# Kernel tuning notes

Hardware: AMD Instinct MI355X
Metric: run time of the kernel (lower is better)

Reference implementation:

```python
import jax, jax.numpy as jnp
import numpy as np

B, W, H, C = 8, 32, 32, 64   # batch, width, height, hidden_size
NH = 8                        # num_attention_heads
M = 32                        # max_position_embeddings
P = C // 2                    # position_embedding_size (query_positional_score=True)


def setup_inputs() -> dict:
    key = jax.random.key(0)
    ks = jax.random.split(key, 7)
    s = 0.02
    return {
        "hidden_states": jax.random.normal(ks[0], (B, W, H, C), dtype=jnp.float32),
        "row_emb": jax.random.normal(ks[1], (2 * M - 1, P), dtype=jnp.float32) * s,
        "col_emb": jax.random.normal(ks[2], (2 * M - 1, P), dtype=jnp.float32) * s,
        "Wq": jax.random.normal(ks[3], (NH * C, C), dtype=jnp.float32) * s,
        "bq": jnp.zeros((NH * C,), dtype=jnp.float32),
        "Wk": jax.random.normal(ks[4], (NH * C, C), dtype=jnp.float32) * s,
        "bk": jnp.zeros((NH * C,), dtype=jnp.float32),
        "Wv": jax.random.normal(ks[5], (C, NH * C), dtype=jnp.float32) * s,
        "bv": jnp.zeros((C,), dtype=jnp.float32),
    }


def reference(hidden_states, row_emb, col_emb, Wq, bq, Wk, bk, Wv, bv):
    b, w, h, c = hidden_states.shape
    nh = Wq.shape[0] // c
    half = c // 2
    center = row_emb.shape[0] // 2  # = max_position_embeddings - 1

    # projections: all_head_size = nh * c (per source: hidden_size * num_heads)
    q = (hidden_states @ Wq.T + bq).reshape(b, w, h, nh, c)
    k = (hidden_states @ Wk.T + bk).reshape(b, w, h, nh, c)

    # relative index tables: rel[i, j] = (j - i) + (M - 1)
    iw = jnp.arange(w)
    ih = jnp.arange(h)
    rel_w = iw[None, :] - iw[:, None] + center   # (w, w)
    rel_h = ih[None, :] - ih[:, None] + center   # (h, h)
    r_emb = row_emb[rel_w]  # (w, w, P)
    c_emb = col_emb[rel_h]  # (h, h, P)

    # positional scores: q split into row/col halves
    q_row = q[..., :half]
    q_col = q[..., half:]
    row_scores = jnp.einsum('bijhd,ikd->bijhk', q_row, r_emb)  # (b,w,h,nh,w)
    col_scores = jnp.einsum('bijhd,jld->bijhl', q_col, c_emb)  # (b,w,h,nh,h)
    scale = jnp.sqrt(jnp.asarray(c, dtype=hidden_states.dtype))
    scores = (row_scores[..., :, None] + col_scores[..., None, :]) / scale  # (b,w,h,nh,w,h)

    # content scores q^T k
    scores = scores + jnp.einsum('bijhd,bklhd->bijhkl', q, k) / scale

    # softmax over merged spatial key dims (k,l)
    probs = jax.nn.softmax(scores.reshape(b, w, h, nh, w * h), axis=-1).reshape(scores.shape)

    # value mixing directly with hidden_states, then output projection
    mixed = jnp.einsum('bijhkl,bkld->bijhd', probs, hidden_states).reshape(b, w, h, nh * c)
    return mixed @ Wv.T + bv
```

## Files before the change

### kernel.cpp

```cpp
#include <hip/hip_runtime.h>
#include <math.h>

typedef __bf16 bf16;
typedef bf16 bf16x2 __attribute__((ext_vector_type(2)));
typedef bf16 bf16x4 __attribute__((ext_vector_type(4)));
typedef bf16 bf16x8 __attribute__((ext_vector_type(8)));
typedef float f32x4 __attribute__((ext_vector_type(4)));

constexpr int CENTER = 31;

static __device__ __forceinline__ unsigned short f2bf_bits(float f) {
    bf16 b = (bf16)f;
    return __builtin_bit_cast(unsigned short, b);
}

__global__ __launch_bounds__(256)
void prep_kernel(const float* __restrict__ hid,
                 const float* __restrict__ Wq, const float* __restrict__ Wk,
                 const float* __restrict__ Wv,
                 bf16* __restrict__ hb, bf16* __restrict__ htb,
                 bf16* __restrict__ Wqb, bf16* __restrict__ Wkb,
                 bf16* __restrict__ Wvp)
{
    __shared__ __attribute__((aligned(16))) bf16 hs[64][72];

    const int t   = threadIdx.x;
    const int blk = blockIdx.x;
    const int b   = blk >> 4, kc = blk & 15;

    {
        int row = t >> 2, c4 = (t & 3) * 16;
        const float4* src = (const float4*)(hid + ((size_t)b * 1024 + kc * 64 + row) * 64 + c4);
        bf16 tmp[16];
        #pragma unroll
        for (int u = 0; u < 4; ++u) {
            float4 v = src[u];
            tmp[4*u+0] = (bf16)v.x; tmp[4*u+1] = (bf16)v.y;
            tmp[4*u+2] = (bf16)v.z; tmp[4*u+3] = (bf16)v.w;
        }
        *(int4*)&hs[row][c4]     = ((int4*)tmp)[0];
        *(int4*)&hs[row][c4 + 8] = ((int4*)tmp)[1];
        bf16* hdst = hb + ((size_t)b * 1024 + kc * 64 + row) * 64 + c4;
        *(int4*)hdst       = ((int4*)tmp)[0];
        *(int4*)(hdst + 8) = ((int4*)tmp)[1];
    }

    {
        int idx = blk * 256 + t;
        if (idx < 8192) {
            float4 vq = ((const float4*)Wq)[idx];
            float4 vk = ((const float4*)Wk)[idx];
            float4 vv = ((const float4*)Wv)[idx];
            ushort4 pq, pk2, pv;
            pq.x = f2bf_bits(vq.x); pq.y = f2bf_bits(vq.y); pq.z = f2bf_bits(vq.z); pq.w = f2bf_bits(vq.w);
            pk2.x = f2bf_bits(vk.x); pk2.y = f2bf_bits(vk.y); pk2.z = f2bf_bits(vk.z); pk2.w = f2bf_bits(vk.w);
            pv.x = f2bf_bits(vv.x); pv.y = f2bf_bits(vv.y); pv.z = f2bf_bits(vv.z); pv.w = f2bf_bits(vv.w);
            ((ushort4*)Wqb)[idx] = pq;
            ((ushort4*)Wkb)[idx] = pk2;
            int c = idx >> 7, o4 = (idx & 127) * 4;
            size_t dst = (size_t)((c >> 4) * 16 + (o4 >> 5)) * 512 + (c & 15) * 32 + (o4 & 31);
            *(ushort4*)(Wvp + dst) = pv;
        }
    }
    __syncthreads();

    {
        int d = t >> 2, p0 = (t & 3) * 16;
        ushort tmp[16];
        #pragma unroll
        for (int i = 0; i < 16; ++i)
            tmp[i] = __builtin_bit_cast(unsigned short, hs[p0 + i][d]);
        bf16* dst = htb + ((size_t)b * 64 + d) * 1024 + kc * 64 + p0;
        *(int4*)dst       = ((int4*)tmp)[0];
        *(int4*)(dst + 8) = ((int4*)tmp)[1];
    }
}

__global__ __launch_bounds__(256)
void qkproj_kernel(const bf16* __restrict__ hb,
                   const bf16* __restrict__ Wqb, const float* __restrict__ bq,
                   const bf16* __restrict__ Wkb, const float* __restrict__ bk,
                   bf16* __restrict__ qb, bf16* __restrict__ kb)
{
    __shared__ __attribute__((aligned(16))) bf16 As[128][72];
    __shared__ __attribute__((aligned(16))) bf16 Bqs[128][72];
    __shared__ __attribute__((aligned(16))) bf16 Bks[128][72];

    const int t  = threadIdx.x;
    const int pt = blockIdx.x;
    const int ot = blockIdx.y;
    const int p0 = pt * 128;
    const int b  = p0 >> 10;

    {
        int row = t >> 1, ch = (t & 1) * 32;
        const int4* asrc = (const int4*)(hb + (size_t)(p0 + row) * 64 + ch);
        const int4* qsrc = (const int4*)(Wqb + (size_t)(ot * 128 + row) * 64 + ch);
        const int4* ksrc = (const int4*)(Wkb + (size_t)(ot * 128 + row) * 64 + ch);
        #pragma unroll
        for (int u = 0; u < 4; ++u) {
            *(int4*)&As[row][ch + u * 8]  = asrc[u];
            *(int4*)&Bqs[row][ch + u * 8] = qsrc[u];
            *(int4*)&Bks[row][ch + u * 8] = ksrc[u];
        }
    }
    __syncthreads();

    const int w = t >> 6, ln = t & 63, l15 = ln & 15, quad = ln >> 4;

    bf16x8 a[2][2];
    #pragma unroll
    for (int mt = 0; mt < 2; ++mt) {
        a[mt][0] = *(const bf16x8*)&As[w * 32 + mt * 16 + l15][quad * 8];
        a[mt][1] = *(const bf16x8*)&As[w * 32 + mt * 16 + l15][32 + quad * 8];
    }

    const f32x4 z4 = {0.f, 0.f, 0.f, 0.f};

    for (int z = 0; z < 2; ++z) {
        const bf16 (* __restrict__ Bs)[72] = z ? Bks : Bqs;
        const float* bias = z ? bk : bq;
        bf16* outp        = z ? kb : qb;
        const float scale = z ? 1.0f : 0.125f;

        f32x4 acc[2][8];
        #pragma unroll
        for (int mt = 0; mt < 2; ++mt)
            #pragma unroll
            for (int nt = 0; nt < 8; ++nt) acc[mt][nt] = z4;

        #pragma unroll
        for (int nt = 0; nt < 8; ++nt) {
            bf16x8 b0 = *(const bf16x8*)&Bs[nt * 16 + l15][quad * 8];
            bf16x8 b1 = *(const bf16x8*)&Bs[nt * 16 + l15][32 + quad * 8];
            #pragma unroll
            for (int mt = 0; mt < 2; ++mt) {
                acc[mt][nt] = __builtin_amdgcn_mfma_f32_16x16x32_bf16(a[mt][0], b0, acc[mt][nt], 0, 0, 0);
                acc[mt][nt] = __builtin_amdgcn_mfma_f32_16x16x32_bf16(a[mt][1], b1, acc[mt][nt], 0, 0, 0);
            }
        }

        #pragma unroll
        for (int nt = 0; nt < 8; ++nt) {
            int o = ot * 128 + nt * 16 + l15;
            float bv = bias[o];
            int hh = o >> 6, d = o & 63;
            #pragma unroll
            for (int mt = 0; mt < 2; ++mt)
                #pragma unroll
                for (int r = 0; r < 4; ++r) {
                    int pos = (p0 & 1023) + w * 32 + mt * 16 + quad * 4 + r;
                    float val = (acc[mt][nt][r] + bv) * scale;
                    outp[(((size_t)b * 8 + hh) * 1024 + pos) * 64 + d] = (bf16)val;
                }
        }
    }
}

__global__ __launch_bounds__(256)
void bias_kernel(const bf16* __restrict__ qb,
                 const float* __restrict__ row_emb, const float* __restrict__ col_emb,
                 bf16* __restrict__ rowbias, bf16* __restrict__ colbias)
{
    __shared__ __attribute__((aligned(16))) bf16 embRs[63][40];
    __shared__ __attribute__((aligned(16))) bf16 embCs[63][40];

    const int t  = threadIdx.x;
    const int bh = blockIdx.x;
    const int sg = blockIdx.y;

    for (int i = t; i < 2016; i += 256) embRs[i >> 5][i & 31] = (bf16)row_emb[i];
    for (int i = t; i < 2016; i += 256) embCs[i >> 5][i & 31] = (bf16)col_emb[i];
    __syncthreads();

    const int w = t >> 6, ln = t & 63, l15 = ln & 15, quad = ln >> 4;

    #pragma unroll
    for (int u = 0; u < 4; ++u) {
        int s = sg * 16 + u * 4 + w;
        bool cm = s >= 32;
        int ij = cm ? s - 32 : s;

        bf16x8 a[2];
        #pragma unroll
        for (int mt = 0; mt < 2; ++mt) {
            const bf16* ap = cm
                ? qb + ((size_t)bh * 1024 + (mt * 16 + l15) * 32 + ij) * 64 + 32 + quad * 8
                : qb + ((size_t)bh * 1024 + ij * 32 + mt * 16 + l15) * 64 + quad * 8;
            a[mt] = *(const bf16x8*)ap;
        }
        bf16* ob = cm ? colbias : rowbias;

        #pragma unroll
        for (int nt = 0; nt < 2; ++nt) {
            int erow = nt * 16 + l15 + CENTER - ij;
            bf16x8 bfrag = cm ? *(const bf16x8*)&embCs[erow][quad * 8]
                              : *(const bf16x8*)&embRs[erow][quad * 8];
            #pragma unroll
            for (int mt = 0; mt < 2; ++mt) {
                f32x4 c = {0.f, 0.f, 0.f, 0.f};
                c = __builtin_amdgcn_mfma_f32_16x16x32_bf16(a[mt], bfrag, c, 0, 0, 0);
                #pragma unroll
                for (int r = 0; r < 4; ++r) {
                    int ql = mt * 16 + quad * 4 + r;
                    int qrow = cm ? ql * 32 + ij : ij * 32 + ql;
                    ob[((size_t)bh * 1024 + qrow) * 32 + nt * 16 + l15] = (bf16)c[r];
                }
            }
        }
    }
}

__global__ __launch_bounds__(256, 2)
void attn_kernel(const bf16* __restrict__ qb, const bf16* __restrict__ kb,
                 const bf16* __restrict__ htb,
                 const bf16* __restrict__ rowbias, const bf16* __restrict__ colbias,
                 bf16* __restrict__ mixedb)
{
    __shared__ __attribute__((aligned(16))) bf16 Ks[64][72];
    __shared__ __attribute__((aligned(16))) bf16 Hts[64][72];
    __shared__ __attribute__((aligned(16))) bf16 Pp[4][32][72];

    const int t  = threadIdx.x;
    const int qt = blockIdx.x;
    const int bh = blockIdx.y;
    const int b  = bh >> 3, h = bh & 7;
    const int q0 = qt * 128;
    const int w = t >> 6, ln = t & 63, l15 = ln & 15, quad = ln >> 4;

    bf16x8 bq_[2][2];
    float  cbv[2][2][4];
    const bf16* rbp[2];
    #pragma unroll
    for (int mt = 0; mt < 2; ++mt) {
        int qrow = q0 + w * 32 + mt * 16 + l15;
        const bf16* qp = qb + ((size_t)bh * 1024 + qrow) * 64;
        bq_[mt][0] = *(const bf16x8*)(qp + quad * 8);
        bq_[mt][1] = *(const bf16x8*)(qp + 32 + quad * 8);
        #pragma unroll
        for (int par = 0; par < 2; ++par) {
            bf16x4 cv = *(const bf16x4*)(colbias + ((size_t)bh * 1024 + qrow) * 32 + par * 16 + quad * 4);
            #pragma unroll
            for (int r = 0; r < 4; ++r) cbv[mt][par][r] = (float)cv[r];
        }
        rbp[mt] = rowbias + ((size_t)bh * 1024 + qrow) * 32;
    }

    const f32x4 z4 = {0.f, 0.f, 0.f, 0.f};
    f32x4 oacc[2][4];
    float lsum[2] = {0.f, 0.f};
    #pragma unroll
    for (int mt = 0; mt < 2; ++mt)
        #pragma unroll
        for (int dt = 0; dt < 4; ++dt) oacc[mt][dt] = z4;

    bf16* Pw = &Pp[w][0][0];
    const bf16* kcbase = kb + (size_t)bh * 1024 * 64;
    const bf16* hcbase = htb + (size_t)b * 64 * 1024;

    for (int kc = 0; kc < 16; ++kc) {
        __syncthreads();
        {
            int row = t >> 2, c = (t & 3) << 4;
            const bf16* ksrc = kcbase + (size_t)(kc * 64 + row) * 64 + c;
            *(int4*)&Ks[row][c]     = *(const int4*)ksrc;
            *(int4*)&Ks[row][c + 8] = *(const int4*)(ksrc + 8);
            const bf16* hsrc = hcbase + (size_t)row * 1024 + kc * 64 + c;
            *(int4*)&Hts[row][c]     = *(const int4*)hsrc;
            *(int4*)&Hts[row][c + 8] = *(const int4*)(hsrc + 8);
        }
        float rb[2][2];
        #pragma unroll
        for (int mt = 0; mt < 2; ++mt) {
            bf16x2 rv = *(const bf16x2*)(rbp[mt] + kc * 2);
            rb[mt][0] = (float)rv[0]; rb[mt][1] = (float)rv[1];
        }
        __syncthreads();

        f32x4 sf[2][4];
        #pragma unroll
        for (int mt = 0; mt < 2; ++mt)
            #pragma unroll
            for (int kt = 0; kt < 4; ++kt) sf[mt][kt] = z4;
        #pragma unroll
        for (int kt = 0; kt < 4; ++kt) {
            bf16x8 aK0 = *(const bf16x8*)&Ks[kt * 16 + l15][quad * 8];
            bf16x8 aK1 = *(const bf16x8*)&Ks[kt * 16 + l15][32 + quad * 8];
            #pragma unroll
            for (int mt = 0; mt < 2; ++mt) {
                sf[mt][kt] = __builtin_amdgcn_mfma_f32_16x16x32_bf16(aK0, bq_[mt][0], sf[mt][kt], 0, 0, 0);
                sf[mt][kt] = __builtin_amdgcn_mfma_f32_16x16x32_bf16(aK1, bq_[mt][1], sf[mt][kt], 0, 0, 0);
            }
        }

        #pragma unroll
        for (int mt = 0; mt < 2; ++mt)
            #pragma unroll
            for (int kt = 0; kt < 4; ++kt) {
                float rbv = rb[mt][kt >> 1];
                ushort4 pk;
                float p0 = __expf(sf[mt][kt][0] + rbv + cbv[mt][kt & 1][0]);
                float p1 = __expf(sf[mt][kt][1] + rbv + cbv[mt][kt & 1][1]);
                float p2 = __expf(sf[mt][kt][2] + rbv + cbv[mt][kt & 1][2]);
                float p3 = __expf(sf[mt][kt][3] + rbv + cbv[mt][kt & 1][3]);
                lsum[mt] += (p0 + p1) + (p2 + p3);
                pk.x = f2bf_bits(p0); pk.y = f2bf_bits(p1);
                pk.z = f2bf_bits(p2); pk.w = f2bf_bits(p3);
                *(ushort4*)&Pw[(mt * 16 + l15) * 72 + kt * 16 + quad * 4] = pk;
            }

        bf16x8 bp[2][2];
        #pragma unroll
        for (int mt = 0; mt < 2; ++mt) {
            bp[mt][0] = *(const bf16x8*)&Pw[(mt * 16 + l15) * 72 + quad * 8];
            bp[mt][1] = *(const bf16x8*)&Pw[(mt * 16 + l15) * 72 + 32 + quad * 8];
        }
        #pragma unroll
        for (int dt = 0; dt < 4; ++dt) {
            bf16x8 aH0 = *(const bf16x8*)&Hts[dt * 16 + l15][quad * 8];
            bf16x8 aH1 = *(const bf16x8*)&Hts[dt * 16 + l15][32 + quad * 8];
            #pragma unroll
            for (int mt = 0; mt < 2; ++mt) {
                oacc[mt][dt] = __builtin_amdgcn_mfma_f32_16x16x32_bf16(aH0, bp[mt][0], oacc[mt][dt], 0, 0, 0);
                oacc[mt][dt] = __builtin_amdgcn_mfma_f32_16x16x32_bf16(aH1, bp[mt][1], oacc[mt][dt], 0, 0, 0);
            }
        }
    }

    float inv[2];
    #pragma unroll
    for (int mt = 0; mt < 2; ++mt) {
        float v = lsum[mt];
        v += __shfl_xor(v, 16);
        v += __shfl_xor(v, 32);
        inv[mt] = 1.0f / v;
    }
    #pragma unroll
    for (int mt = 0; mt < 2; ++mt) {
        int pos = q0 + w * 32 + mt * 16 + l15;
        bf16* mb = mixedb + ((size_t)b * 1024 + pos) * 512 + h * 64;
        #pragma unroll
        for (int dt = 0; dt < 4; ++dt) {
            ushort4 pk;
            pk.x = f2bf_bits(oacc[mt][dt][0] * inv[mt]);
            pk.y = f2bf_bits(oacc[mt][dt][1] * inv[mt]);
            pk.z = f2bf_bits(oacc[mt][dt][2] * inv[mt]);
            pk.w = f2bf_bits(oacc[mt][dt][3] * inv[mt]);
            *(ushort4*)(mb + dt * 16 + quad * 4) = pk;
        }
    }
}

__global__ __launch_bounds__(256)
void out_proj_kernel(const bf16* __restrict__ mixedb,
                     const bf16* __restrict__ Wvp, const float* __restrict__ bv,
                     float* __restrict__ out)
{
    const int t  = threadIdx.x;
    const int p0 = blockIdx.x * 32;
    const int w = t >> 6, ln = t & 63, l15 = ln & 15, quad = ln >> 4;

    float bvv = bv[w * 16 + l15];
    f32x4 acc[2] = {(f32x4){bvv, bvv, bvv, bvv}, (f32x4){bvv, bvv, bvv, bvv}};

    const bf16* arow0 = mixedb + (size_t)(p0 + l15) * 512 + quad * 8;
    const bf16* arow1 = mixedb + (size_t)(p0 + 16 + l15) * 512 + quad * 8;
    const bf16* bbase = Wvp + (size_t)w * 16 * 512 + l15 * 32 + quad * 8;

    #pragma unroll
    for (int kc = 0; kc < 16; ++kc) {
        bf16x8 a0 = *(const bf16x8*)(arow0 + kc * 32);
        bf16x8 a1 = *(const bf16x8*)(arow1 + kc * 32);
        bf16x8 bfrag = *(const bf16x8*)(bbase + kc * 512);
        acc[0] = __builtin_amdgcn_mfma_f32_16x16x32_bf16(a0, bfrag, acc[0], 0, 0, 0);
        acc[1] = __builtin_amdgcn_mfma_f32_16x16x32_bf16(a1, bfrag, acc[1], 0, 0, 0);
    }

    #pragma unroll
    for (int mt = 0; mt < 2; ++mt)
        #pragma unroll
        for (int r = 0; r < 4; ++r)
            out[(size_t)(p0 + mt * 16 + quad * 4 + r) * 64 + w * 16 + l15] = acc[mt][r];
}

extern "C" void kernel_launch(void* const* d_in, const int* in_sizes, int n_in,
                              void* d_out, int out_size, void* d_ws, size_t ws_size,
                              hipStream_t stream)
{
    const float* hid     = (const float*)d_in[0];
    const float* row_emb = (const float*)d_in[1];
    const float* col_emb = (const float*)d_in[2];
    const float* Wq      = (const float*)d_in[3];
    const float* bq      = (const float*)d_in[4];
    const float* Wk      = (const float*)d_in[5];
    const float* bk      = (const float*)d_in[6];
    const float* Wv      = (const float*)d_in[7];
    const float* bv      = (const float*)d_in[8];
    float* out = (float*)d_out;

    bf16* qb      = (bf16*)d_ws;
    bf16* kb      = qb + (size_t)64 * 1024 * 64;
    bf16* htb     = kb + (size_t)64 * 1024 * 64;
    bf16* rowbias = htb + (size_t)8 * 64 * 1024;
    bf16* colbias = rowbias + (size_t)64 * 1024 * 32;
    bf16* mixedb  = colbias + (size_t)64 * 1024 * 32;
    bf16* hb      = mixedb + (size_t)8 * 1024 * 512;
    bf16* Wqb     = hb + (size_t)8 * 1024 * 64;
    bf16* Wkb     = Wqb + (size_t)512 * 64;
    bf16* Wvp     = Wkb + (size_t)512 * 64;

    prep_kernel<<<128, 256, 0, stream>>>(hid, Wq, Wk, Wv, hb, htb, Wqb, Wkb, Wvp);
    qkproj_kernel<<<dim3(64, 4), 256, 0, stream>>>(hb, Wqb, bq, Wkb, bk, qb, kb);
    bias_kernel<<<dim3(64, 4), 256, 0, stream>>>(qb, row_emb, col_emb, rowbias, colbias);
    attn_kernel<<<dim3(8, 64), 256, 0, stream>>>(qb, kb, htb, rowbias, colbias, mixedb);
    out_proj_kernel<<<256, 256, 0, stream>>>(mixedb, Wvp, bv, out);
}
```

Before: 129.2 us.

## Prefetch next K/H tile into registers, use exp2 with folded log2e, set MFMA priority

The attention loop now loads the next chunk of K, transposed hidden states and row bias into registers during the current iteration, so global load latency overlaps with the MFMA and softmax work. The query scale folds in log2(e), which lets exp be replaced by the hardware exp2 instruction. s_setprio raises wave priority around the MFMA blocks. The costs are higher register pressure and a dependence on the row/col biases also being in the log2 domain; if they were not rescaled, the results would be incorrect.

```diff
diff --git a/kernel.cpp b/kernel.cpp
--- a/kernel.cpp
+++ b/kernel.cpp
@@ -8,10 +8,19 @@
 typedef float f32x4 __attribute__((ext_vector_type(4)));
 
 constexpr int CENTER = 31;
+constexpr float QSCALE = 0.125f * 1.4426950408889634f;
 
 static __device__ __forceinline__ unsigned short f2bf_bits(float f) {
     bf16 b = (bf16)f;
     return __builtin_bit_cast(unsigned short, b);
+}
+
+static __device__ __forceinline__ float fast_exp2(float x) {
+#if __has_builtin(__builtin_amdgcn_exp2f)
+    return __builtin_amdgcn_exp2f(x);
+#else
+    return exp2f(x);
+#endif
 }
 
 __global__ __launch_bounds__(256)
@@ -121,7 +130,7 @@
         const bf16 (* __restrict__ Bs)[72] = z ? Bks : Bqs;
         const float* bias = z ? bk : bq;
         bf16* outp        = z ? kb : qb;
-        const float scale = z ? 1.0f : 0.125f;
+        const float scale = z ? 1.0f : QSCALE;
 
         f32x4 acc[2][8];
         #pragma unroll
@@ -258,30 +267,50 @@
     const bf16* kcbase = kb + (size_t)bh * 1024 * 64;
     const bf16* hcbase = htb + (size_t)b * 64 * 1024;
 
+    const int srow = t >> 2, sc = (t & 3) << 4;
+    const bf16* kptr = kcbase + (size_t)srow * 64 + sc;
+    const bf16* hptr = hcbase + (size_t)srow * 1024 + sc;
+
+    int4 kr0 = *(const int4*)(kptr);
+    int4 kr1 = *(const int4*)(kptr + 8);
+    int4 hr0 = *(const int4*)(hptr);
+    int4 hr1 = *(const int4*)(hptr + 8);
+    bf16x2 rnext[2];
+    #pragma unroll
+    for (int mt = 0; mt < 2; ++mt) rnext[mt] = *(const bf16x2*)(rbp[mt]);
+
     for (int kc = 0; kc < 16; ++kc) {
         __syncthreads();
-        {
-            int row = t >> 2, c = (t & 3) << 4;
-            const bf16* ksrc = kcbase + (size_t)(kc * 64 + row) * 64 + c;
-            *(int4*)&Ks[row][c]     = *(const int4*)ksrc;
-            *(int4*)&Ks[row][c + 8] = *(const int4*)(ksrc + 8);
-            const bf16* hsrc = hcbase + (size_t)row * 1024 + kc * 64 + c;
-            *(int4*)&Hts[row][c]     = *(const int4*)hsrc;
-            *(int4*)&Hts[row][c + 8] = *(const int4*)(hsrc + 8);
-        }
+        *(int4*)&Ks[srow][sc]      = kr0;
+        *(int4*)&Ks[srow][sc + 8]  = kr1;
+        *(int4*)&Hts[srow][sc]     = hr0;
+        *(int4*)&Hts[srow][sc + 8] = hr1;
         float rb[2][2];
         #pragma unroll
         for (int mt = 0; mt < 2; ++mt) {
-            bf16x2 rv = *(const bf16x2*)(rbp[mt] + kc * 2);
-            rb[mt][0] = (float)rv[0]; rb[mt][1] = (float)rv[1];
+            rb[mt][0] = (float)rnext[mt][0];
+            rb[mt][1] = (float)rnext[mt][1];
         }
         __syncthreads();
 
+        if (kc < 15) {
+            const bf16* kn = kptr + (size_t)(kc + 1) * 4096;
+            const bf16* hn = hptr + (size_t)(kc + 1) * 64;
+            kr0 = *(const int4*)(kn);
+            kr1 = *(const int4*)(kn + 8);
+            hr0 = *(const int4*)(hn);
+            hr1 = *(const int4*)(hn + 8);
+            #pragma unroll
+            for (int mt = 0; mt < 2; ++mt)
+                rnext[mt] = *(const bf16x2*)(rbp[mt] + (kc + 1) * 2);
+        }
+
         f32x4 sf[2][4];
         #pragma unroll
         for (int mt = 0; mt < 2; ++mt)
             #pragma unroll
             for (int kt = 0; kt < 4; ++kt) sf[mt][kt] = z4;
+        __builtin_amdgcn_s_setprio(1);
         #pragma unroll
         for (int kt = 0; kt < 4; ++kt) {
             bf16x8 aK0 = *(const bf16x8*)&Ks[kt * 16 + l15][quad * 8];
@@ -292,6 +321,7 @@
                 sf[mt][kt] = __builtin_amdgcn_mfma_f32_16x16x32_bf16(aK1, bq_[mt][1], sf[mt][kt], 0, 0, 0);
             }
         }
+        __builtin_amdgcn_s_setprio(0);
 
         #pragma unroll
         for (int mt = 0; mt < 2; ++mt)
@@ -299,10 +329,10 @@
             for (int kt = 0; kt < 4; ++kt) {
                 float rbv = rb[mt][kt >> 1];
                 ushort4 pk;
-                float p0 = __expf(sf[mt][kt][0] + rbv + cbv[mt][kt & 1][0]);
-                float p1 = __expf(sf[mt][kt][1] + rbv + cbv[mt][kt & 1][1]);
-                float p2 = __expf(sf[mt][kt][2] + rbv + cbv[mt][kt & 1][2]);
-                float p3 = __expf(sf[mt][kt][3] + rbv + cbv[mt][kt & 1][3]);
+                float p0 = fast_exp2(sf[mt][kt][0] + rbv + cbv[mt][kt & 1][0]);
+                float p1 = fast_exp2(sf[mt][kt][1] + rbv + cbv[mt][kt & 1][1]);
+                float p2 = fast_exp2(sf[mt][kt][2] + rbv + cbv[mt][kt & 1][2]);
+                float p3 = fast_exp2(sf[mt][kt][3] + rbv + cbv[mt][kt & 1][3]);
                 lsum[mt] += (p0 + p1) + (p2 + p3);
                 pk.x = f2bf_bits(p0); pk.y = f2bf_bits(p1);
                 pk.z = f2bf_bits(p2); pk.w = f2bf_bits(p3);
@@ -315,6 +345,7 @@
             bp[mt][0] = *(const bf16x8*)&Pw[(mt * 16 + l15) * 72 + quad * 8];
             bp[mt][1] = *(const bf16x8*)&Pw[(mt * 16 + l15) * 72 + 32 + quad * 8];
         }
+        __builtin_amdgcn_s_setprio(1);
         #pragma unroll
         for (int dt = 0; dt < 4; ++dt) {
             bf16x8 aH0 = *(const bf16x8*)&Hts[dt * 16 + l15][quad * 8];
@@ -325,6 +356,7 @@
                 oacc[mt][dt] = __builtin_amdgcn_mfma_f32_16x16x32_bf16(aH1, bp[mt][1], oacc[mt][dt], 0, 0, 0);
             }
         }
+        __builtin_amdgcn_s_setprio(0);
     }
 
     float inv[2];
```

Measured after the change: 125.5 us. 2.9% less time.
